# Kernel optimization log

Measured on AMD Instinct MI355X. Metric: run time of the kernel, lower is better.

Reference implementation:

```python
import jax, jax.numpy as jnp
import numpy as np
import math

HEADS, DIM_HEAD, LANDMARKS, PINV_ITERS = 8, 64, 256, 6
EMB = 512


def layer_norm(x, g, b, eps=1e-5):
    mu = jnp.mean(x, -1, keepdims=True)
    var = jnp.mean((x - mu) ** 2, -1, keepdims=True)
    return (x - mu) / jnp.sqrt(var + eps) * g + b


def moore_penrose_pinv(x, iters=PINV_ITERS):
    # iterative Moore-Penrose pseudo-inverse (lucidrains nystrom-attention)
    abs_x = jnp.abs(x)
    col = abs_x.sum(-1)
    row = abs_x.sum(-2)
    z = jnp.swapaxes(x, -1, -2) / (jnp.max(col) * jnp.max(row))
    I = jnp.eye(x.shape[-1], dtype=x.dtype)
    for _ in range(iters):
        xz = x @ z
        z = 0.25 * z @ (13.0 * I - xz @ (15.0 * I - xz @ (7.0 * I - xz)))
    return z


def dw_seq_conv(v, w):
    # v: [b, h, n, d]; depthwise Conv2d(heads, heads, (33,1), pad (16,0), groups=heads)
    return jax.lax.conv_general_dilated(
        v, w, (1, 1), ((w.shape[2] // 2, w.shape[2] // 2), (0, 0)),
        dimension_numbers=('NCHW', 'OIHW', 'NCHW'), feature_group_count=v.shape[1])


def nystrom_attention(x, qkv_w, out_w, out_b, res_w):
    b, n, _ = x.shape
    m = LANDMARKS
    pad = (m - n % m) % m
    if pad:
        x = jnp.pad(x, ((0, 0), (pad, 0), (0, 0)))  # front-pad like F.pad(..., padding, 0)
    n_p = n + pad
    qkv = x @ qkv_w  # [b, n_p, 3*h*dh]
    q, k, v = jnp.split(qkv, 3, axis=-1)
    to_h = lambda t: t.reshape(b, n_p, HEADS, DIM_HEAD).transpose(0, 2, 1, 3)
    q, k, v = to_h(q), to_h(k), to_h(v)
    q = q * (DIM_HEAD ** -0.5)
    l = n_p // m  # tokens per landmark
    q_l = q.reshape(b, HEADS, m, l, DIM_HEAD).mean(3)
    k_l = k.reshape(b, HEADS, m, l, DIM_HEAD).mean(3)
    a1 = jax.nn.softmax(jnp.einsum('bhid,bhjd->bhij', q, k_l), -1)    # [b,h,n_p,m]
    a2 = jax.nn.softmax(jnp.einsum('bhid,bhjd->bhij', q_l, k_l), -1)  # [b,h,m,m]
    a3 = jax.nn.softmax(jnp.einsum('bhid,bhjd->bhij', q_l, k), -1)    # [b,h,m,n_p]
    a2_inv = moore_penrose_pinv(a2)
    out = (a1 @ a2_inv) @ (a3 @ v)  # [b,h,n_p,dh]
    out = out + dw_seq_conv(v, res_w)  # residual depthwise conv on v
    out = out.transpose(0, 2, 1, 3).reshape(b, n_p, HEADS * DIM_HEAD)
    out = out @ out_w + out_b
    return out[:, -n:]


def ppeg(x, H, W, w7, b7, w5, b5, w3, b3):
    B, _, C = x.shape
    cls_t, feat = x[:, :1], x[:, 1:]
    f = feat.transpose(0, 2, 1).reshape(B, C, H, W)
    def dw(w, b):
        y = jax.lax.conv_general_dilated(
            f, w, (1, 1), 'SAME', dimension_numbers=('NCHW', 'OIHW', 'NCHW'),
            feature_group_count=C)
        return y + b[None, :, None, None]
    y = f + dw(w7, b7) + dw(w5, b5) + dw(w3, b3)
    y = y.reshape(B, C, H * W).transpose(0, 2, 1)
    return jnp.concatenate([cls_t, y], axis=1)


def setup_inputs():
    key = jax.random.key(0)
    ks = jax.random.split(key, 20)
    rn = lambda k, shp, s=0.02: jax.random.normal(k, shp, jnp.float32) * s
    return {
        'x_path': jax.random.normal(ks[0], (4, 6000, 1024), jnp.float32),
        'fc1_w': rn(ks[1], (1024, EMB)), 'fc1_b': jnp.zeros((EMB,), jnp.float32),
        'cls_token': jax.random.normal(ks[2], (1, 1, EMB), jnp.float32),
        'ln1_g': jnp.ones((EMB,), jnp.float32), 'ln1_b': jnp.zeros((EMB,), jnp.float32),
        'qkv1_w': rn(ks[3], (EMB, 3 * HEADS * DIM_HEAD)),
        'out1_w': rn(ks[4], (HEADS * DIM_HEAD, EMB)), 'out1_b': jnp.zeros((EMB,), jnp.float32),
        'res1_w': rn(ks[5], (HEADS, 1, 33, 1)),
        'ln2_g': jnp.ones((EMB,), jnp.float32), 'ln2_b': jnp.zeros((EMB,), jnp.float32),
        'qkv2_w': rn(ks[6], (EMB, 3 * HEADS * DIM_HEAD)),
        'out2_w': rn(ks[7], (HEADS * DIM_HEAD, EMB)), 'out2_b': jnp.zeros((EMB,), jnp.float32),
        'res2_w': rn(ks[8], (HEADS, 1, 33, 1)),
        'conv7_w': rn(ks[9], (EMB, 1, 7, 7)), 'conv7_b': jnp.zeros((EMB,), jnp.float32),
        'conv5_w': rn(ks[10], (EMB, 1, 5, 5)), 'conv5_b': jnp.zeros((EMB,), jnp.float32),
        'conv3_w': rn(ks[11], (EMB, 1, 3, 3)), 'conv3_b': jnp.zeros((EMB,), jnp.float32),
        'norm_g': jnp.ones((EMB,), jnp.float32), 'norm_b': jnp.zeros((EMB,), jnp.float32),
        'fc2_w': rn(ks[12], (EMB, 4)), 'fc2_b': jnp.zeros((4,), jnp.float32),
    }


def reference(x_path, fc1_w, fc1_b, cls_token, ln1_g, ln1_b, qkv1_w, out1_w, out1_b,
              res1_w, ln2_g, ln2_b, qkv2_w, out2_w, out2_b, res2_w,
              conv7_w, conv7_b, conv5_w, conv5_b, conv3_w, conv3_b,
              norm_g, norm_b, fc2_w, fc2_b):
    h = jax.nn.relu(x_path @ fc1_w + fc1_b)  # [B, N, EMB]
    B, N = h.shape[0], h.shape[1]
    _H = int(math.ceil(math.sqrt(N)))
    add = _H * _H - N
    h = jnp.concatenate([h, h[:, :add]], axis=1)            # square padding
    cls = jnp.broadcast_to(cls_token, (B, 1, EMB))
    h = jnp.concatenate([cls, h], axis=1)                   # [B, _H*_H+1, EMB]
    # TransLayer 1
    h = h + nystrom_attention(layer_norm(h, ln1_g, ln1_b), qkv1_w, out1_w, out1_b, res1_w)
    # PPEG positional encoding
    h = ppeg(h, _H, _H, conv7_w, conv7_b, conv5_w, conv5_b, conv3_w, conv3_b)
    # TransLayer 2
    h = h + nystrom_attention(layer_norm(h, ln2_g, ln2_b), qkv2_w, out2_w, out2_b, res2_w)
    h = layer_norm(h, norm_g, norm_b)
    logits = h @ fc2_w + fc2_b
    cls_logit = logits[:, 0]
    Y_hat = jnp.argmax(cls_logit, axis=1)
    hazards = jax.nn.sigmoid(cls_logit)
    S = jnp.cumprod(1.0 - hazards, axis=1)
    return hazards, S, Y_hat
```

## Files before the change

### kernel.cpp

```cpp
#include <hip/hip_runtime.h>
#include <math.h>

namespace {

constexpr int Bq   = 4;
constexpr int N0   = 6000;
constexpr int KIN  = 1024;
constexpr int E    = 512;
constexpr int HH   = 78;
constexpr int HWp  = 6084;
constexpr int N1   = 6085;
constexpr int NH   = 8;
constexpr int DH   = 64;
constexpr int LM   = 256;
constexpr int NP   = 6144;
constexpr int LCH  = 24;
constexpr int PADS = 59;
constexpr int BH   = Bq * NH;
constexpr int QKV  = 3 * E;
constexpr int NSPL = 8;

typedef __attribute__((ext_vector_type(8))) short bf16x8;
typedef __attribute__((ext_vector_type(4))) float f32x4;

// ... 140 lines not shown
          float vv = (wch == 0) ? v * 0.125f : v;
          unsigned short* dst = (wch == 0) ? qp : (wch == 1) ? kp : vp;
          dst[(((size_t)(b * NH + hd)) * NP + p) * DH + d] = f2bf(vv);
        } else if (STORE == 1) {
          C[((size_t)(row / N0) * N1 + 1 + (row % N0)) * N + col] = v;
        } else if (STORE == 3) {
          C[(size_t)row * N + col] += v;
        } else {
          C[(size_t)row * N + col] = v;
        }
      }
    }
  }
}

template<bool WN, bool WT, bool TBF>
__global__ __launch_bounds__(256)
void mm_ns(const float* __restrict__ A, const float* __restrict__ BT,
           float* __restrict__ Cn, unsigned short* __restrict__ CtB,
           float* __restrict__ CtF, int Ncols, int Mtot, int K,
           long long sA, long long sBT, long long sCn, long long sCt,
           float cN, float aN, float cT, float aT)
{
  int bx = blockIdx.x, by = blockIdx.y, bz = blockIdx.z;
  {
    const int gx = gridDim.x, gy = gridDim.y;
    int nid = xcd_swz((bz * gy + by) * gx + bx, gx * gy * gridDim.z);
    bx = nid % gx; nid /= gx; by = nid % gy; bz = nid / gy;
  }
  A  += (size_t)bz * sA;
  BT += (size_t)bz * sBT;
  __shared__ __align__(16) char smem[32768];
  unsigned short* Ah = (unsigned short*)smem;
  unsigned short* Al = Ah + 4096;
  unsigned short* Bh = Ah + 8192;
  unsigned short* Bl = Ah + 12288;
  const int t = threadIdx.x, lane = t & 63, w = t >> 6;
  const int l15 = lane & 15, g = lane >> 4;
  const int rb = by * 64, cb = bx * 64;
  const int wr = w * 16;

  f32x4 acc[4];
  #pragma unroll
  for (int ni = 0; ni < 4; ni++) acc[ni] = (f32x4){0.f, 0.f, 0.f, 0.f};

  for (int k0 = 0; k0 < K; k0 += 64) {
    if (k0) __syncthreads();
    #pragma unroll
    for (int it = 0; it < 4; it++) {
      const int id = it * 256 + t;
      const int row = id >> 4, kq = (id & 15) * 4;
      float4 va = *reinterpret_cast<const float4*>(A + (size_t)(rb + row) * K + k0 + kq);
      const int eo = row * 64 + swz8(row, kq >> 3) * 8 + (kq & 7);
      unsigned short h0 = f2bf(va.x), h1 = f2bf(va.y), h2 = f2bf(va.z), h3 = f2bf(va.w);
      unsigned short lo0 = f2bf(va.x - bf2f(h0)), lo1 = f2bf(va.y - bf2f(h1));
      unsigned short lo2 = f2bf(va.z - bf2f(h2)), lo3 = f2bf(va.w - bf2f(h3));
      *reinterpret_cast<ushort4*>(&Ah[eo]) = make_ushort4(h0, h1, h2, h3);
      *reinterpret_cast<ushort4*>(&Al[eo]) = make_ushort4(lo0, lo1, lo2, lo3);
      float4 vb = *reinterpret_cast<const float4*>(BT + (size_t)(cb + row) * K + k0 + kq);
      unsigned short b0 = f2bf(vb.x), b1 = f2bf(vb.y), b2 = f2bf(vb.z), b3 = f2bf(vb.w);
      unsigned short c0_ = f2bf(vb.x - bf2f(b0)), c1 = f2bf(vb.y - bf2f(b1));
      unsigned short c2 = f2bf(vb.z - bf2f(b2)), c3 = f2bf(vb.w - bf2f(b3));
      *reinterpret_cast<ushort4*>(&Bh[eo]) = make_ushort4(b0, b1, b2, b3);
      *reinterpret_cast<ushort4*>(&Bl[eo]) = make_ushort4(c0_, c1, c2, c3);
    }
    __syncthreads();
    #pragma unroll
    for (int ds = 0; ds < 2; ds++) {
      const int ar = wr + l15;
      bf16x8 ah = *reinterpret_cast<const bf16x8*>(&Ah[ar * 64 + swz8(ar, ds * 4 + g) * 8]);
      bf16x8 al = *reinterpret_cast<const bf16x8*>(&Al[ar * 64 + swz8(ar, ds * 4 + g) * 8]);
      #pragma unroll
      for (int ni = 0; ni < 4; ni++) {
        const int nr = ni * 16 + l15;
        bf16x8 bhf = *reinterpret_cast<const bf16x8*>(&Bh[nr * 64 + swz8(nr, ds * 4 + g) * 8]);
        bf16x8 blf = *reinterpret_cast<const bf16x8*>(&Bl[nr * 64 + swz8(nr, ds * 4 + g) * 8]);
        acc[ni] = __builtin_amdgcn_mfma_f32_16x16x32_bf16(ah, bhf, acc[ni], 0, 0, 0);
        acc[ni] = __builtin_amdgcn_mfma_f32_16x16x32_bf16(ah, blf, acc[ni], 0, 0, 0);
        acc[ni] = __builtin_amdgcn_mfma_f32_16x16x32_bf16(al, bhf, acc[ni], 0, 0, 0);
      }
    }
  }
  __syncthreads();
  float* tb = (float*)smem;
  #pragma unroll
  for (int ni = 0; ni < 4; ni++)
    #pragma unroll
    for (int r = 0; r < 4; r++)
      tb[(wr + g * 4 + r) * 65 + l15 + ni * 16] = acc[ni][r];
  __syncthreads();
  #pragma unroll
  for (int it = 0; it < 4; it++) {
    const int id = it * 256 + t;
    const int row = id >> 4, q4 = (id & 15) * 4;
    if (WN) {
      float4 o;
      #pragma unroll
      for (int j = 0; j < 4; j++) {
        float v = tb[row * 65 + q4 + j];
        ((float*)&o)[j] = ((rb + row) == (cb + q4 + j) ? cN : 0.f) + aN * v;
      }
      *reinterpret_cast<float4*>(Cn + (size_t)bz * sCn + (size_t)(rb + row) * Ncols + cb + q4) = o;
    }
    if (WT) {
      float v[4];
      #pragma unroll
      for (int j = 0; j < 4; j++) {
        float m = tb[(q4 + j) * 65 + row];
        v[j] = ((cb + row) == (rb + q4 + j) ? cT : 0.f) + aT * m;
      }
      if (TBF) {
        ushort4 o = make_ushort4(f2bf(v[0]), f2bf(v[1]), f2bf(v[2]), f2bf(v[3]));
        *reinterpret_cast<ushort4*>(CtB + (size_t)bz * sCt + (size_t)(cb + row) * Mtot + rb + q4) = o;
      } else {
        float4 o = make_float4(v[0], v[1], v[2], v[3]);
        *reinterpret_cast<float4*>(CtF + (size_t)bz * sCt + (size_t)(cb + row) * Mtot + rb + q4) = o;
      }
    }
  }
}

__global__ __launch_bounds__(256)
void a2_fused(const unsigned short* __restrict__ ql, const unsigned short* __restrict__ kl,
              float* __restrict__ a2, float* __restrict__ a2T)
{
  const int bh = blockIdx.y;
  const int t = threadIdx.x, lane = t & 63, w = t >> 6;
  const int l15 = lane & 15, g = lane >> 4;
  const int row0 = blockIdx.x * 64 + w * 16;
  __shared__ float tb[4][16][68];

  bf16x8 af[2];
// ... 147 lines not shown
  for (int r = 0; r < 4; r++) {
    const int row = lm0 + w * 16 + g * 4 + r;
    const size_t base = ((size_t)(bh * NSPL + sp) * LM + row);
    #pragma unroll
    for (int ni = 0; ni < 4; ni++)
      Opart[base * 64 + ni * 16 + l15] = O[ni][r];
    if (l15 == 0) {
      msd[base * 2]     = m[r];
      msd[base * 2 + 1] = sd[r];
    }
  }
}

__global__ __launch_bounds__(256)
void flash_a3_merge(const float* __restrict__ Opart, const float* __restrict__ msd,
                    float* __restrict__ a3vT)
{
  const int bh = blockIdx.y, lm0 = blockIdx.x * 64;
  const int t = threadIdx.x;
  const int r = t >> 2, dg = t & 3;
  const int row = lm0 + r;
  float m8[NSPL], w8[NSPL];
  float M = -INFINITY;
  #pragma unroll
  for (int s = 0; s < NSPL; s++) {
    m8[s] = msd[((size_t)(bh * NSPL + s) * LM + row) * 2];
    M = fmaxf(M, m8[s]);
  }
  float S = 0.f;
  #pragma unroll
  for (int s = 0; s < NSPL; s++) {
// ... 7 lines not shown
  for (int j = 0; j < 16; j++) acc[j] = 0.f;
  #pragma unroll
  for (int s = 0; s < NSPL; s++) {
    const float* op = Opart + ((size_t)(bh * NSPL + s) * LM + row) * 64 + dg * 16;
    #pragma unroll
    for (int j = 0; j < 16; j++) acc[j] = fmaf(w8[s], op[j], acc[j]);
  }
  __shared__ float Tl[64][65];
  #pragma unroll
  for (int j = 0; j < 16; j++) Tl[dg * 16 + j][r] = acc[j] * invS;
  __syncthreads();
  const int d = t >> 2, q4 = t & 3;
  #pragma unroll
  for (int j = 0; j < 4; j++) {
    const int c0 = q4 * 16 + j * 4;
    float4 o = make_float4(Tl[d][c0], Tl[d][c0 + 1], Tl[d][c0 + 2], Tl[d][c0 + 3]);
    *reinterpret_cast<float4*>(a3vT + ((size_t)bh * 64 + d) * 256 + lm0 + c0) = o;
  }
}

__global__ __launch_bounds__(256)
void a1_fused(const unsigned short* __restrict__ q, const unsigned short* __restrict__ kl,
              const unsigned short* __restrict__ W2T, const unsigned short* __restrict__ v,
              const float* __restrict__ resw, unsigned short* __restrict__ heads)
{
  const int bh = blockIdx.y;
  const int p0 = blockIdx.x * 64;
  const int t = threadIdx.x, lane = t & 63, w = t >> 6;
  const int l15 = lane & 15, g = lane >> 4;
  __shared__ __align__(16) unsigned short Pl[4][4096];
  __shared__ __align__(16) unsigned short VTc[8192];
  __shared__ __align__(16) unsigned short P2[8192];

  const float* w33 = resw + (bh & 7) * 33;
  for (int i = t; i < 64 * 96; i += 256) {
    const int r = i / 96, kk = i % 96;
    const int d = kk - r;
    const float val = (d >= 0 && d <= 32) ? w33[d] : 0.f;
    P2[r * 128 + swz8(r, kk >> 3) * 8 + (kk & 7)] = f2bf(val);
  }
  #pragma unroll
  for (int it = 0; it < 3; it++) {
    const int id = it * 256 + t;
    const int kp = id >> 3, ch = id & 7;
    const int gp = p0 - 16 + kp;
    int4 vv = make_int4(0, 0, 0, 0);
    if (gp >= 0 && gp < NP)
      vv = *reinterpret_cast<const int4*>(v + ((size_t)bh * NP + gp) * 64 + ch * 8);
    const unsigned short* ps = (const unsigned short*)&vv;
    #pragma unroll
    for (int j = 0; j < 8; j++) {
      const int d = ch * 8 + j;
      VTc[d * 128 + swz8(d, kp >> 3) * 8 + (kp & 7)] = ps[j];
    }
  }
// ... 17 lines not shown
  for (int r = 0; r < 4; r++) {
    float m = -INFINITY;
    #pragma unroll
    for (int ni = 0; ni < 16; ni++) m = fmaxf(m, s[ni][r]);
    #pragma unroll
    for (int msk = 1; msk < 16; msk <<= 1) m = fmaxf(m, __shfl_xor(m, msk));
    float sm = 0.f;
    #pragma unroll
    for (int ni = 0; ni < 16; ni++) { float e = expf(s[ni][r] - m); s[ni][r] = e; sm += e; }
    #pragma unroll
    for (int msk = 1; msk < 16; msk <<= 1) sm += __shfl_xor(sm, msk);
    const float inv = 1.f / sm;
    #pragma unroll
    for (int ni = 0; ni < 16; ni++) s[ni][r] *= inv;
  }
  unsigned short* Pw = Pl[w];
  #pragma unroll
  for (int ni = 0; ni < 16; ni++)
    #pragma unroll
    for (int r = 0; r < 4; r++) {
      const int rowl = g * 4 + r, col = ni * 16 + l15;
      Pw[rowl * 256 + swz8(rowl, col >> 3) * 8 + (col & 7)] = f2bf(s[ni][r]);
    }
  f32x4 O[4];
  #pragma unroll
  for (int ni = 0; ni < 4; ni++) O[ni] = (f32x4){0.f, 0.f, 0.f, 0.f};
  #pragma unroll
  for (int ks = 0; ks < 8; ks++) {
    bf16x8 pa = *reinterpret_cast<const bf16x8*>(&Pw[l15 * 256 + swz8(l15, ks * 4 + g) * 8]);
    #pragma unroll
    for (int ni = 0; ni < 4; ni++) {
      bf16x8 bf = *reinterpret_cast<const bf16x8*>(
          W2T + ((size_t)bh * 64 + ni * 16 + l15) * 256 + ks * 32 + g * 8);
      O[ni] = __builtin_amdgcn_mfma_f32_16x16x32_bf16(pa, bf, O[ni], 0, 0, 0);
    }
  }
  #pragma unroll
  for (int ks = 0; ks < 3; ks++) {
    const int ar = w * 16 + l15;
    bf16x8 pa = *reinterpret_cast<const bf16x8*>(&P2[ar * 128 + swz8(ar, ks * 4 + g) * 8]);
    #pragma unroll
    for (int ni = 0; ni < 4; ni++) {
      const int d = ni * 16 + l15;
      bf16x8 bv = *reinterpret_cast<const bf16x8*>(&VTc[d * 128 + swz8(d, ks * 4 + g) * 8]);
      O[ni] = __builtin_amdgcn_mfma_f32_16x16x32_bf16(pa, bv, O[ni], 0, 0, 0);
    }
  }
  #pragma unroll
  for (int ni = 0; ni < 4; ni++)
    #pragma unroll
    for (int r = 0; r < 4; r++)
      heads[((size_t)bh * NP + p0 + w * 16 + g * 4 + r) * 64 + ni * 16 + l15] = f2bf(O[ni][r]);
}

__global__ __launch_bounds__(256)
void ln_stats(const float* __restrict__ X, float* __restrict__ stats)
{
  const size_t row = blockIdx.x;
  const float* x = X + row * E;
  const int tid = threadIdx.x;
  float2 v = *reinterpret_cast<const float2*>(x + tid * 2);
  __shared__ float red[256];
  red[tid] = v.x + v.y;
  __syncthreads();
  for (int s = 128; s > 0; s >>= 1) { if (tid < s) red[tid] += red[tid + s]; __syncthreads(); }
  const float mu = red[0] * (1.f / E);
  __syncthreads();
  const float dx = v.x - mu, dy = v.y - mu;
  red[tid] = dx * dx + dy * dy;
  __syncthreads();
  for (int s = 128; s > 0; s >>= 1) { if (tid < s) red[tid] += red[tid + s]; __syncthreads(); }
  if (tid == 0) {
    stats[2 * row]     = mu;
    stats[2 * row + 1] = 1.f / sqrtf(red[0] * (1.f / E) + 1e-5f);
  }
}

__global__ __launch_bounds__(256)
void ln_to_bf16(const float* __restrict__ h, const float* __restrict__ stats,
                const float* __restrict__ g, const float* __restrict__ b,
                unsigned short* __restrict__ xb)
{
  long long idx = (long long)blockIdx.x * 256 + threadIdx.x;
  const long long total = (long long)Bq * N1 * (E / 4);
  if (idx >= total) return;
  const int e4 = (int)(idx % (E / 4));
  const long long row = idx / (E / 4);
  float4 hx = reinterpret_cast<const float4*>(h)[idx];
  const float mu = stats[2 * row], inv = stats[2 * row + 1];
  float4 gg = reinterpret_cast<const float4*>(g)[e4];
  float4 bb = reinterpret_cast<const float4*>(b)[e4];
  ushort4 o;
  o.x = f2bf((hx.x - mu) * inv * gg.x + bb.x);
  o.y = f2bf((hx.y - mu) * inv * gg.y + bb.y);
  o.z = f2bf((hx.z - mu) * inv * gg.z + bb.z);
  o.w = f2bf((hx.w - mu) * inv * gg.w + bb.w);
  reinterpret_cast<ushort4*>(xb)[idx] = o;
}

__global__ void fill_cls_wrap(const float* __restrict__ cls, float* __restrict__ h)
{
  int idx = blockIdx.x * 256 + threadIdx.x;
  const int total = Bq * 85 * (E / 4);
  if (idx >= total) return;
  const int e4 = idx % (E / 4);
  int t = idx / (E / 4);
  const int rr = t % 85;
  const int b = t / 85;
  float4* H = reinterpret_cast<float4*>(h);
  if (rr == 0) {
    H[((size_t)b * N1) * (E / 4) + e4] = reinterpret_cast<const float4*>(cls)[e4];
  } else {
    const int i = rr - 1;
    H[((size_t)b * N1 + 1 + N0 + i) * (E / 4) + e4] =
        H[((size_t)b * N1 + 1 + i) * (E / 4) + e4];
  }
}

__global__ __launch_bounds__(256)
void landmark_mean(const float* __restrict__ h, const float* __restrict__ stats,
                   const float* __restrict__ g, const float* __restrict__ bta,
                   unsigned short* __restrict__ xl)
{
  const int bm = blockIdx.x;
  const int b = bm / LM, i = bm % LM;
  const int tid = threadIdx.x;
  float2 acc = make_float2(0.f, 0.f);
  float cnt = 0.f;
  for (int j = 0; j < LCH; j++) {
    const int real = i * LCH + j - PADS;
    if (real < 0) continue;
    const size_t row = (size_t)b * N1 + real;
    float2 hv = *reinterpret_cast<const float2*>(h + row * E + tid * 2);
    const float mu = stats[2 * row], inv = stats[2 * row + 1];
    acc.x += (hv.x - mu) * inv;
    acc.y += (hv.y - mu) * inv;
    cnt += 1.f;
  }
  float2 gg = *reinterpret_cast<const float2*>(g + tid * 2);
  float2 bb = *reinterpret_cast<const float2*>(bta + tid * 2);
  ushort2 o;
  o.x = f2bf((gg.x * acc.x + bb.x * cnt) * (1.f / LCH));
  o.y = f2bf((gg.y * acc.y + bb.y * cnt) * (1.f / LCH));
  *reinterpret_cast<ushort2*>(xl + (size_t)bm * E + tid * 2) = o;
}

__global__ void zero_pad_rows(unsigned short* __restrict__ q, unsigned short* __restrict__ k,
                              unsigned short* __restrict__ v)
{
  const int idx = blockIdx.x * 256 + threadIdx.x;
  const int total = BH * PADS * DH;
  if (idx >= total) return;
  const int d = idx % DH;
  int t = idx / DH;
  const int p = t % PADS;
  const int bh = t / PADS;
  const size_t o = ((size_t)bh * NP + p) * DH + d;
  q[o] = 0; k[o] = 0; v[o] = 0;
// ... 30 lines not shown
  for (int j = 0; j < LM; j++) rowsum += a[(size_t)tid * LM + j];
  for (int i = 0; i < LM; i++) colsum += a[(size_t)i * LM + tid];
  __shared__ float r1[256], r2[256];
  r1[tid] = rowsum; r2[tid] = colsum;
  __syncthreads();
  for (int s = 128; s > 0; s >>= 1) {
    if (tid < s) { r1[tid] = fmaxf(r1[tid], r1[tid + s]); r2[tid] = fmaxf(r2[tid], r2[tid + s]); }
    __syncthreads();
  }
  if (tid == 0) {
    atomicMax(&gmax[0], __float_as_uint(r1[0]));
    atomicMax(&gmax[1], __float_as_uint(r2[0]));
  }
}

__global__ void pinv_init2(const float* __restrict__ a2, const float* __restrict__ a2T,
                           const unsigned int* __restrict__ gmax,
                           float* __restrict__ zA, float* __restrict__ zAT)
{
  long long idx = (long long)blockIdx.x * 256 + threadIdx.x;
  const long long total = (long long)BH * LM * LM;
  if (idx >= total) return;
  const float inv = 1.f / (__uint_as_float(gmax[0]) * __uint_as_float(gmax[1]));
  zA[idx]  = a2T[idx] * inv;
  zAT[idx] = a2[idx] * inv;
}

__global__ __launch_bounds__(256)
void last_row_attn(const unsigned short* __restrict__ q, const unsigned short* __restrict__ kl,
                   const unsigned short* __restrict__ W2T, const unsigned short* __restrict__ v,
                   const float* __restrict__ resw, float* __restrict__ hb)
{
  const int bh = blockIdx.x;
  const int tid = threadIdx.x;
  __shared__ float qrow[DH];
  __shared__ float p[LM];
  __shared__ float red[256];
  if (tid < DH) qrow[tid] = bf2f(q[((size_t)bh * NP + PADS) * DH + tid]);
  __syncthreads();
  const unsigned short* krow = kl + ((size_t)bh * LM + tid) * DH;
// ... 199 lines not shown
    for (int j = 1; j < 4; j++) if (lg[j] > bvv) { bvv = lg[j]; best = j; }
    float S = 1.f;
    for (int j = 0; j < 4; j++) {
      const float hz = 1.f / (1.f + expf(-lg[j]));
      out[b * 4 + j] = hz;
      S *= (1.f - hz);
      out[16 + b * 4 + j] = S;
    }
    out[32 + b] = (float)best;
  }
}

__global__ void write_sentinel(float* out) { if (threadIdx.x < 36) out[threadIdx.x] = -777.f; }

struct Ws {
  unsigned short *q, *k, *v, *ql, *kl, *xl, *W2T;
  unsigned short *fc1T, *qkv1T, *qkv2T, *out1T;
  float *h, *pool, *a3vT, *qkvl, *stats;
  unsigned int* gmax;
};

constexpr long long MM = (long long)BH * LM * LM;

static void run_attention(hipStream_t stream, Ws& w,
                          const float* lng, const float* lnb, const unsigned short* qkvT,
                          const unsigned short* outT, const float* outb, const float* resw,
                          bool last)
{
  const dim3 blk(256);
  float* a2   = w.pool;
  float* a2T  = w.pool + MM;
  float* zA   = w.pool + 2 * MM;
  float* zAT  = w.pool + 3 * MM;
  float* zB   = w.pool + 4 * MM;
  float* zBT  = w.pool + 5 * MM;
  float* Y    = w.pool + 6 * MM;
  float* P1T  = w.pool + 7 * MM;
  float* P2T  = w.pool + 8 * MM;
  float* P3T  = w.pool + 9 * MM;
  unsigned short* xb    = (unsigned short*)w.pool;
  unsigned short* heads = (unsigned short*)(w.pool + 6 * MM);
  float* Opart = w.pool + 6 * MM;
  float* msd   = w.pool + 6 * MM + (long long)BH * NSPL * LM * DH;
  float* hb = w.qkvl;

  ln_stats<<<Bq * N1, blk, 0, stream>>>(w.h, w.stats);
  ln_to_bf16<<<gblocks_i((long long)Bq * N1 * (E / 4)), blk, 0, stream>>>(w.h, w.stats, lng, lnb, xb);
  landmark_mean<<<Bq * LM, blk, 0, stream>>>(w.h, w.stats, lng, lnb, w.xl);
  mgemm<3, 2, false, false, true><<<dim3(QKV / 128, (Bq * N1 + 127) / 128), blk, 0, stream>>>(
      xb, qkvT, nullptr, nullptr, w.q, w.k, w.v, nullptr, Bq * N1, QKV, E);
  zero_pad_rows<<<gblocks_i((long long)BH * PADS * DH), blk, 0, stream>>>(w.q, w.k, w.v);
  mgemm<3, 0, false, false, false><<<dim3(8, 8), blk, 0, stream>>>(
      w.xl, qkvT, nullptr, w.qkvl, nullptr, nullptr, nullptr, nullptr, Bq * LM, 1024, E);
  scatter_qk_l<<<gblocks_i((long long)Bq * LM * 256), blk, 0, stream>>>(w.qkvl, w.ql, w.kl);

  a2_fused<<<dim3(4, BH), blk, 0, stream>>>(w.ql, w.kl, a2, a2T);
  init_gmax<<<1, 64, 0, stream>>>(w.gmax);
  colrow_max<<<BH, blk, 0, stream>>>(a2, w.gmax);
  pinv_init2<<<gblocks_i(MM), blk, 0, stream>>>(a2, a2T, w.gmax, zA, zAT);

  float *zc = zA, *zcT = zAT, *zo = zB, *zoT = zBT;
  const long long sM = (long long)LM * LM;
  for (int it = 0; it < 6; ++it) {
    mm_ns<true, true, false><<<dim3(4, 4, BH), blk, 0, stream>>>(
        a2, zcT, Y, nullptr, P1T, 256, 256, 256, sM, sM, sM, sM, 0.f, 1.f, 7.f, -1.f);
    mm_ns<false, true, false><<<dim3(4, 4, BH), blk, 0, stream>>>(
        Y, P1T, nullptr, nullptr, P2T, 256, 256, 256, sM, sM, sM, sM, 0.f, 0.f, 15.f, -1.f);
    mm_ns<false, true, false><<<dim3(4, 4, BH), blk, 0, stream>>>(
        Y, P2T, nullptr, nullptr, P3T, 256, 256, 256, sM, sM, sM, sM, 0.f, 0.f, 13.f, -1.f);
    mm_ns<true, true, false><<<dim3(4, 4, BH), blk, 0, stream>>>(
        zc, P3T, zo, nullptr, zoT, 256, 256, 256, sM, sM, sM, sM, 0.f, 0.25f, 0.f, 0.25f);
    float* t1 = zc; zc = zo; zo = t1;
    float* t2 = zcT; zcT = zoT; zoT = t2;
  }

  flash_a3_split<<<dim3(4, NSPL, BH), blk, 0, stream>>>(w.ql, w.k, w.v, Opart, msd);
  flash_a3_merge<<<dim3(4, BH), blk, 0, stream>>>(Opart, msd, w.a3vT);
  mm_ns<false, true, true><<<dim3(1, 4, BH), blk, 0, stream>>>(
      zc, w.a3vT, nullptr, w.W2T, nullptr, 64, 256, 256, sM, 64 * 256, 0, 64 * 256,
      0.f, 0.f, 0.f, 1.f);

  if (!last) {
    a1_fused<<<dim3(NP / 64, BH), blk, 0, stream>>>(w.q, w.kl, w.W2T, w.v, resw, heads);
    mgemm<4, 3, true, false, true><<<dim3(E / 128, (Bq * N1 + 127) / 128), blk, 0, stream>>>(
        nullptr, outT, outb, w.h, nullptr, nullptr, nullptr, heads, Bq * N1, E, E);
  } else {
    last_row_attn<<<BH, blk, 0, stream>>>(w.q, w.kl, w.W2T, w.v, resw, hb);
  }
}

}

extern "C" void kernel_launch(void* const* d_in, const int* in_sizes, int n_in,
                              void* d_out, int out_size, void* d_ws, size_t ws_size,
                              hipStream_t stream)
{
  const float* x_path   = (const float*)d_in[0];
  const float* fc1_w    = (const float*)d_in[1];
  const float* fc1_b    = (const float*)d_in[2];
  const float* cls_tok  = (const float*)d_in[3];
  const float* ln1_g    = (const float*)d_in[4];
  const float* ln1_b    = (const float*)d_in[5];
// ... 21 lines not shown

  float* W = (float*)d_ws;
  size_t off = 0;
  auto take = [&](size_t n) -> float* {
    float* p = W + off;
    off += (n + 255) & ~(size_t)255;
    return p;
  };

  Ws w;
  w.q     = (unsigned short*)take((size_t)BH * NP * DH / 2);
  w.k     = (unsigned short*)take((size_t)BH * NP * DH / 2);
  w.v     = (unsigned short*)take((size_t)BH * NP * DH / 2);
  w.h     = take((size_t)Bq * N1 * E);
  w.pool  = take((size_t)10 * MM);
  w.a3vT  = take((size_t)BH * DH * LM);
  w.W2T   = (unsigned short*)take((size_t)BH * DH * LM / 2);
  w.ql    = (unsigned short*)take((size_t)BH * LM * DH / 2);
  w.kl    = (unsigned short*)take((size_t)BH * LM * DH / 2);
  w.xl    = (unsigned short*)take((size_t)Bq * LM * E / 2);
  w.qkvl  = take((size_t)Bq * LM * 1024);
  w.stats = take((size_t)2 * Bq * N1);
  w.fc1T  = (unsigned short*)take((size_t)E * KIN / 2);
  w.qkv1T = (unsigned short*)take((size_t)QKV * E / 2);
  w.qkv2T = (unsigned short*)take((size_t)QKV * E / 2);
  w.out1T = (unsigned short*)take((size_t)E * E / 2);
  w.gmax  = (unsigned int*)take(64);

  if (ws_size < off * sizeof(float)) {
    write_sentinel<<<1, 64, 0, stream>>>((float*)d_out);
    return;
  }

  const dim3 blk(256);

  wcvt_t<<<dim3(E / 32, KIN / 32), blk, 0, stream>>>(fc1_w, w.fc1T, KIN, E);
  wcvt_t<<<dim3(QKV / 32, E / 32), blk, 0, stream>>>(qkv1_w, w.qkv1T, E, QKV);
// ... 23 lines not shown
```

Baseline: 1.931 ms.

## Store pinv matrices as pre-split bf16 hi/lo pairs and fuse layernorm passes

The Newton-Schulz pinv matmuls now read and write matrices already split into bf16 high/low halves, so the fp32-to-bf16 split in every tile load is gone and global traffic is smaller. LayerNorm stats and the bf16 conversion are merged into one kernel, and landmark means are taken from the normalized bf16 output rather than recomputed from fp32. a1_fused loads its depthwise-conv band matrix from a buffer built once per layer, and writes its P tile to shared memory in two halves, cutting LDS use and possibly raising occupancy. Taking landmark means from rounded bf16 values slightly changes numerics.

Measured after the change: 1.830 ms. 5.2% less time.

```diff
diff --git a/kernel.cpp b/kernel.cpp
--- a/kernel.cpp
+++ b/kernel.cpp
@@ -178,13 +178,15 @@
   }
 }
 
-template<bool WN, bool WT, bool TBF>
-__global__ __launch_bounds__(256)
-void mm_ns(const float* __restrict__ A, const float* __restrict__ BT,
-           float* __restrict__ Cn, unsigned short* __restrict__ CtB,
-           float* __restrict__ CtF, int Ncols, int Mtot, int K,
-           long long sA, long long sBT, long long sCn, long long sCt,
-           float cN, float aN, float cT, float aT)
+template<bool WN, bool WT>
+__global__ __launch_bounds__(256)
+void mm_ns2(const unsigned short* __restrict__ Ah, const unsigned short* __restrict__ Al,
+            const unsigned short* __restrict__ Bth, const unsigned short* __restrict__ Btl,
+            unsigned short* __restrict__ Cnh, unsigned short* __restrict__ Cnl,
+            unsigned short* __restrict__ Cth, unsigned short* __restrict__ Ctl,
+            int Ncols, int Mtot, int K,
+            long long sA, long long sB, long long sCn, long long sCt,
+            float cN, float aN, float cT, float aT)
 {
   int bx = blockIdx.x, by = blockIdx.y, bz = blockIdx.z;
   {
@@ -192,13 +194,15 @@
     int nid = xcd_swz((bz * gy + by) * gx + bx, gx * gy * gridDim.z);
     bx = nid % gx; nid /= gx; by = nid % gy; bz = nid / gy;
   }
-  A  += (size_t)bz * sA;
-  BT += (size_t)bz * sBT;
+  const unsigned short* Ahb = Ah + (size_t)bz * sA;
+  const unsigned short* Alb = Al + (size_t)bz * sA;
+  const unsigned short* Bhb = Bth + (size_t)bz * sB;
+  const unsigned short* Blb = Btl + (size_t)bz * sB;
   __shared__ __align__(16) char smem[32768];
-  unsigned short* Ah = (unsigned short*)smem;
-  unsigned short* Al = Ah + 4096;
-  unsigned short* Bh = Ah + 8192;
-  unsigned short* Bl = Ah + 12288;
+  unsigned short* AhS = (unsigned short*)smem;
+  unsigned short* AlS = AhS + 4096;
+  unsigned short* BhS = AhS + 8192;
+  unsigned short* BlS = AhS + 12288;
   const int t = threadIdx.x, lane = t & 63, w = t >> 6;
   const int l15 = lane & 15, g = lane >> 4;
   const int rb = by * 64, cb = bx * 64;
@@ -211,34 +215,28 @@
   for (int k0 = 0; k0 < K; k0 += 64) {
     if (k0) __syncthreads();
     #pragma unroll
-    for (int it = 0; it < 4; it++) {
+    for (int it = 0; it < 2; it++) {
       const int id = it * 256 + t;
-      const int row = id >> 4, kq = (id & 15) * 4;
-      float4 va = *reinterpret_cast<const float4*>(A + (size_t)(rb + row) * K + k0 + kq);
-      const int eo = row * 64 + swz8(row, kq >> 3) * 8 + (kq & 7);
-      unsigned short h0 = f2bf(va.x), h1 = f2bf(va.y), h2 = f2bf(va.z), h3 = f2bf(va.w);
-      unsigned short lo0 = f2bf(va.x - bf2f(h0)), lo1 = f2bf(va.y - bf2f(h1));
-      unsigned short lo2 = f2bf(va.z - bf2f(h2)), lo3 = f2bf(va.w - bf2f(h3));
-      *reinterpret_cast<ushort4*>(&Ah[eo]) = make_ushort4(h0, h1, h2, h3);
-      *reinterpret_cast<ushort4*>(&Al[eo]) = make_ushort4(lo0, lo1, lo2, lo3);
-      float4 vb = *reinterpret_cast<const float4*>(BT + (size_t)(cb + row) * K + k0 + kq);
-      unsigned short b0 = f2bf(vb.x), b1 = f2bf(vb.y), b2 = f2bf(vb.z), b3 = f2bf(vb.w);
-      unsigned short c0_ = f2bf(vb.x - bf2f(b0)), c1 = f2bf(vb.y - bf2f(b1));
-      unsigned short c2 = f2bf(vb.z - bf2f(b2)), c3 = f2bf(vb.w - bf2f(b3));
-      *reinterpret_cast<ushort4*>(&Bh[eo]) = make_ushort4(b0, b1, b2, b3);
-      *reinterpret_cast<ushort4*>(&Bl[eo]) = make_ushort4(c0_, c1, c2, c3);
+      const int row = id >> 3, ch = id & 7;
+      const int eo = row * 64 + swz8(row, ch) * 8;
+      const size_t ga = (size_t)(rb + row) * K + k0 + ch * 8;
+      const size_t gb = (size_t)(cb + row) * K + k0 + ch * 8;
+      *reinterpret_cast<int4*>(&AhS[eo]) = *reinterpret_cast<const int4*>(Ahb + ga);
+      *reinterpret_cast<int4*>(&AlS[eo]) = *reinterpret_cast<const int4*>(Alb + ga);
+      *reinterpret_cast<int4*>(&BhS[eo]) = *reinterpret_cast<const int4*>(Bhb + gb);
+      *reinterpret_cast<int4*>(&BlS[eo]) = *reinterpret_cast<const int4*>(Blb + gb);
     }
     __syncthreads();
     #pragma unroll
     for (int ds = 0; ds < 2; ds++) {
       const int ar = wr + l15;
-      bf16x8 ah = *reinterpret_cast<const bf16x8*>(&Ah[ar * 64 + swz8(ar, ds * 4 + g) * 8]);
-      bf16x8 al = *reinterpret_cast<const bf16x8*>(&Al[ar * 64 + swz8(ar, ds * 4 + g) * 8]);
+      bf16x8 ah = *reinterpret_cast<const bf16x8*>(&AhS[ar * 64 + swz8(ar, ds * 4 + g) * 8]);
+      bf16x8 al = *reinterpret_cast<const bf16x8*>(&AlS[ar * 64 + swz8(ar, ds * 4 + g) * 8]);
       #pragma unroll
       for (int ni = 0; ni < 4; ni++) {
         const int nr = ni * 16 + l15;
-        bf16x8 bhf = *reinterpret_cast<const bf16x8*>(&Bh[nr * 64 + swz8(nr, ds * 4 + g) * 8]);
-        bf16x8 blf = *reinterpret_cast<const bf16x8*>(&Bl[nr * 64 + swz8(nr, ds * 4 + g) * 8]);
+        bf16x8 bhf = *reinterpret_cast<const bf16x8*>(&BhS[nr * 64 + swz8(nr, ds * 4 + g) * 8]);
+        bf16x8 blf = *reinterpret_cast<const bf16x8*>(&BlS[nr * 64 + swz8(nr, ds * 4 + g) * 8]);
         acc[ni] = __builtin_amdgcn_mfma_f32_16x16x32_bf16(ah, bhf, acc[ni], 0, 0, 0);
         acc[ni] = __builtin_amdgcn_mfma_f32_16x16x32_bf16(ah, blf, acc[ni], 0, 0, 0);
         acc[ni] = __builtin_amdgcn_mfma_f32_16x16x32_bf16(al, bhf, acc[ni], 0, 0, 0);
@@ -258,28 +256,30 @@
     const int id = it * 256 + t;
     const int row = id >> 4, q4 = (id & 15) * 4;
     if (WN) {
-      float4 o;
+      ushort4 oh, ol;
       #pragma unroll
       for (int j = 0; j < 4; j++) {
-        float v = tb[row * 65 + q4 + j];
-        ((float*)&o)[j] = ((rb + row) == (cb + q4 + j) ? cN : 0.f) + aN * v;
-      }
-      *reinterpret_cast<float4*>(Cn + (size_t)bz * sCn + (size_t)(rb + row) * Ncols + cb + q4) = o;
+        const float v = ((rb + row) == (cb + q4 + j) ? cN : 0.f) + aN * tb[row * 65 + q4 + j];
+        const unsigned short h = f2bf(v);
+        ((unsigned short*)&oh)[j] = h;
+        ((unsigned short*)&ol)[j] = f2bf(v - bf2f(h));
+      }
+      const size_t o = (size_t)bz * sCn + (size_t)(rb + row) * Ncols + cb + q4;
+      *reinterpret_cast<ushort4*>(Cnh + o) = oh;
+      *reinterpret_cast<ushort4*>(Cnl + o) = ol;
     }
     if (WT) {
-      float v[4];
+      ushort4 oh, ol;
       #pragma unroll
       for (int j = 0; j < 4; j++) {
-        float m = tb[(q4 + j) * 65 + row];
-        v[j] = ((cb + row) == (rb + q4 + j) ? cT : 0.f) + aT * m;
-      }
-      if (TBF) {
-        ushort4 o = make_ushort4(f2bf(v[0]), f2bf(v[1]), f2bf(v[2]), f2bf(v[3]));
-        *reinterpret_cast<ushort4*>(CtB + (size_t)bz * sCt + (size_t)(cb + row) * Mtot + rb + q4) = o;
-      } else {
-        float4 o = make_float4(v[0], v[1], v[2], v[3]);
-        *reinterpret_cast<float4*>(CtF + (size_t)bz * sCt + (size_t)(cb + row) * Mtot + rb + q4) = o;
-      }
+        const float v = ((cb + row) == (rb + q4 + j) ? cT : 0.f) + aT * tb[(q4 + j) * 65 + row];
+        const unsigned short h = f2bf(v);
+        ((unsigned short*)&oh)[j] = h;
+        ((unsigned short*)&ol)[j] = f2bf(v - bf2f(h));
+      }
+      const size_t o = (size_t)bz * sCt + (size_t)(cb + row) * Mtot + rb + q4;
+      *reinterpret_cast<ushort4*>(Cth + o) = oh;
+      *reinterpret_cast<ushort4*>(Ctl + o) = ol;
     }
   }
 }
@@ -457,7 +457,7 @@
 
 __global__ __launch_bounds__(256)
 void flash_a3_merge(const float* __restrict__ Opart, const float* __restrict__ msd,
-                    float* __restrict__ a3vT)
+                    unsigned short* __restrict__ a3vTh, unsigned short* __restrict__ a3vTl)
 {
   const int bh = blockIdx.y, lm0 = blockIdx.x * 64;
   const int t = threadIdx.x;
@@ -495,31 +495,44 @@
   #pragma unroll
   for (int j = 0; j < 4; j++) {
     const int c0 = q4 * 16 + j * 4;
-    float4 o = make_float4(Tl[d][c0], Tl[d][c0 + 1], Tl[d][c0 + 2], Tl[d][c0 + 3]);
-    *reinterpret_cast<float4*>(a3vT + ((size_t)bh * 64 + d) * 256 + lm0 + c0) = o;
+    ushort4 oh, ol;
+    #pragma unroll
+    for (int jj = 0; jj < 4; jj++) {
+      const float v = Tl[d][c0 + jj];
+      const unsigned short h = f2bf(v);
+      ((unsigned short*)&oh)[jj] = h;
+      ((unsigned short*)&ol)[jj] = f2bf(v - bf2f(h));
+    }
+    const size_t o = ((size_t)bh * 64 + d) * 256 + lm0 + c0;
+    *reinterpret_cast<ushort4*>(a3vTh + o) = oh;
+    *reinterpret_cast<ushort4*>(a3vTl + o) = ol;
+  }
+}
+
+__global__ __launch_bounds__(256)
+void build_band(const float* __restrict__ resw, unsigned short* __restrict__ P2g)
+{
+  const int head = blockIdx.x;
+  const float* w33 = resw + head * 33;
+  for (int i = threadIdx.x; i < 64 * 96; i += 256) {
+    const int r = i / 96, kk = i % 96;
+    const int d = kk - r;
+    P2g[(size_t)head * 64 * 96 + i] = f2bf((d >= 0 && d <= 32) ? w33[d] : 0.f);
   }
 }
 
 __global__ __launch_bounds__(256)
 void a1_fused(const unsigned short* __restrict__ q, const unsigned short* __restrict__ kl,
               const unsigned short* __restrict__ W2T, const unsigned short* __restrict__ v,
-              const float* __restrict__ resw, unsigned short* __restrict__ heads)
+              const unsigned short* __restrict__ P2g, unsigned short* __restrict__ heads)
 {
   const int bh = blockIdx.y;
   const int p0 = blockIdx.x * 64;
   const int t = threadIdx.x, lane = t & 63, w = t >> 6;
   const int l15 = lane & 15, g = lane >> 4;
-  __shared__ __align__(16) unsigned short Pl[4][4096];
   __shared__ __align__(16) unsigned short VTc[8192];
-  __shared__ __align__(16) unsigned short P2[8192];
-
-  const float* w33 = resw + (bh & 7) * 33;
-  for (int i = t; i < 64 * 96; i += 256) {
-    const int r = i / 96, kk = i % 96;
-    const int d = kk - r;
-    const float val = (d >= 0 && d <= 32) ? w33[d] : 0.f;
-    P2[r * 128 + swz8(r, kk >> 3) * 8 + (kk & 7)] = f2bf(val);
-  }
+  __shared__ __align__(16) unsigned short Pl[4][2048];
+
   #pragma unroll
   for (int it = 0; it < 3; it++) {
     const int id = it * 256 + t;
@@ -567,31 +580,39 @@
     #pragma unroll
     for (int ni = 0; ni < 16; ni++) s[ni][r] *= inv;
   }
+
+  f32x4 O[4];
+  #pragma unroll
+  for (int ni = 0; ni < 4; ni++) O[ni] = (f32x4){0.f, 0.f, 0.f, 0.f};
   unsigned short* Pw = Pl[w];
   #pragma unroll
-  for (int ni = 0; ni < 16; ni++)
-    #pragma unroll
-    for (int r = 0; r < 4; r++) {
-      const int rowl = g * 4 + r, col = ni * 16 + l15;
-      Pw[rowl * 256 + swz8(rowl, col >> 3) * 8 + (col & 7)] = f2bf(s[ni][r]);
-    }
-  f32x4 O[4];
-  #pragma unroll
-  for (int ni = 0; ni < 4; ni++) O[ni] = (f32x4){0.f, 0.f, 0.f, 0.f};
-  #pragma unroll
-  for (int ks = 0; ks < 8; ks++) {
-    bf16x8 pa = *reinterpret_cast<const bf16x8*>(&Pw[l15 * 256 + swz8(l15, ks * 4 + g) * 8]);
-    #pragma unroll
-    for (int ni = 0; ni < 4; ni++) {
-      bf16x8 bf = *reinterpret_cast<const bf16x8*>(
-          W2T + ((size_t)bh * 64 + ni * 16 + l15) * 256 + ks * 32 + g * 8);
-      O[ni] = __builtin_amdgcn_mfma_f32_16x16x32_bf16(pa, bf, O[ni], 0, 0, 0);
-    }
-  }
+  for (int hf = 0; hf < 2; hf++) {
+    #pragma unroll
+    for (int ni2 = 0; ni2 < 8; ni2++)
+      #pragma unroll
+      for (int r = 0; r < 4; r++) {
+        const int rowl = g * 4 + r, col = ni2 * 16 + l15;
+        Pw[rowl * 128 + swz8(rowl, col >> 3) * 8 + (col & 7)] = f2bf(s[hf * 8 + ni2][r]);
+      }
+    __asm__ __volatile__("" ::: "memory");
+    #pragma unroll
+    for (int ks2 = 0; ks2 < 4; ks2++) {
+      const int ks = hf * 4 + ks2;
+      bf16x8 pa = *reinterpret_cast<const bf16x8*>(&Pw[l15 * 128 + swz8(l15, ks2 * 4 + g) * 8]);
+      #pragma unroll
+      for (int ni = 0; ni < 4; ni++) {
+        bf16x8 bf = *reinterpret_cast<const bf16x8*>(
+            W2T + ((size_t)bh * 64 + ni * 16 + l15) * 256 + ks * 32 + g * 8);
+        O[ni] = __builtin_amdgcn_mfma_f32_16x16x32_bf16(pa, bf, O[ni], 0, 0, 0);
+      }
+    }
+    __asm__ __volatile__("" ::: "memory");
+  }
+  const unsigned short* band = P2g + (size_t)(bh & 7) * 64 * 96;
   #pragma unroll
   for (int ks = 0; ks < 3; ks++) {
     const int ar = w * 16 + l15;
-    bf16x8 pa = *reinterpret_cast<const bf16x8*>(&P2[ar * 128 + swz8(ar, ks * 4 + g) * 8]);
+    bf16x8 pa = *reinterpret_cast<const bf16x8*>(band + (size_t)ar * 96 + ks * 32 + g * 8);
     #pragma unroll
     for (int ni = 0; ni < 4; ni++) {
       const int d = ni * 16 + l15;
@@ -607,7 +628,8 @@
 }
 
 __global__ __launch_bounds__(256)
-void ln_stats(const float* __restrict__ X, float* __restrict__ stats)
+void ln_fused(const float* __restrict__ X, const float* __restrict__ g,
+              const float* __restrict__ b, unsigned short* __restrict__ xb)
 {
   const size_t row = blockIdx.x;
   const float* x = X + row * E;
@@ -623,32 +645,13 @@
   red[tid] = dx * dx + dy * dy;
   __syncthreads();
   for (int s = 128; s > 0; s >>= 1) { if (tid < s) red[tid] += red[tid + s]; __syncthreads(); }
-  if (tid == 0) {
-    stats[2 * row]     = mu;
-    stats[2 * row + 1] = 1.f / sqrtf(red[0] * (1.f / E) + 1e-5f);
-  }
-}
-
-__global__ __launch_bounds__(256)
-void ln_to_bf16(const float* __restrict__ h, const float* __restrict__ stats,
-                const float* __restrict__ g, const float* __restrict__ b,
-                unsigned short* __restrict__ xb)
-{
-  long long idx = (long long)blockIdx.x * 256 + threadIdx.x;
-  const long long total = (long long)Bq * N1 * (E / 4);
-  if (idx >= total) return;
-  const int e4 = (int)(idx % (E / 4));
-  const long long row = idx / (E / 4);
-  float4 hx = reinterpret_cast<const float4*>(h)[idx];
-  const float mu = stats[2 * row], inv = stats[2 * row + 1];
-  float4 gg = reinterpret_cast<const float4*>(g)[e4];
-  float4 bb = reinterpret_cast<const float4*>(b)[e4];
-  ushort4 o;
-  o.x = f2bf((hx.x - mu) * inv * gg.x + bb.x);
-  o.y = f2bf((hx.y - mu) * inv * gg.y + bb.y);
-  o.z = f2bf((hx.z - mu) * inv * gg.z + bb.z);
-  o.w = f2bf((hx.w - mu) * inv * gg.w + bb.w);
-  reinterpret_cast<ushort4*>(xb)[idx] = o;
+  const float inv = 1.f / sqrtf(red[0] * (1.f / E) + 1e-5f);
+  float2 gg = *reinterpret_cast<const float2*>(g + tid * 2);
+  float2 bb = *reinterpret_cast<const float2*>(b + tid * 2);
+  ushort2 o;
+  o.x = f2bf(dx * inv * gg.x + bb.x);
+  o.y = f2bf(dy * inv * gg.y + bb.y);
+  *reinterpret_cast<ushort2*>(xb + row * E + tid * 2) = o;
 }
 
 __global__ void fill_cls_wrap(const float* __restrict__ cls, float* __restrict__ h)
@@ -671,30 +674,22 @@
 }
 
 __global__ __launch_bounds__(256)
-void landmark_mean(const float* __restrict__ h, const float* __restrict__ stats,
-                   const float* __restrict__ g, const float* __restrict__ bta,
-                   unsigned short* __restrict__ xl)
+void landmark_mean(const unsigned short* __restrict__ xb, unsigned short* __restrict__ xl)
 {
   const int bm = blockIdx.x;
   const int b = bm / LM, i = bm % LM;
   const int tid = threadIdx.x;
   float2 acc = make_float2(0.f, 0.f);
-  float cnt = 0.f;
   for (int j = 0; j < LCH; j++) {
     const int real = i * LCH + j - PADS;
     if (real < 0) continue;
-    const size_t row = (size_t)b * N1 + real;
-    float2 hv = *reinterpret_cast<const float2*>(h + row * E + tid * 2);
-    const float mu = stats[2 * row], inv = stats[2 * row + 1];
-    acc.x += (hv.x - mu) * inv;
-    acc.y += (hv.y - mu) * inv;
-    cnt += 1.f;
-  }
-  float2 gg = *reinterpret_cast<const float2*>(g + tid * 2);
-  float2 bb = *reinterpret_cast<const float2*>(bta + tid * 2);
+    ushort2 hv = *reinterpret_cast<const ushort2*>(xb + ((size_t)b * N1 + real) * E + tid * 2);
+    acc.x += bf2f(hv.x);
+    acc.y += bf2f(hv.y);
+  }
   ushort2 o;
-  o.x = f2bf((gg.x * acc.x + bb.x * cnt) * (1.f / LCH));
-  o.y = f2bf((gg.y * acc.y + bb.y * cnt) * (1.f / LCH));
+  o.x = f2bf(acc.x * (1.f / LCH));
+  o.y = f2bf(acc.y * (1.f / LCH));
   *reinterpret_cast<ushort2*>(xl + (size_t)bm * E + tid * 2) = o;
 }
 
@@ -755,16 +750,25 @@
   }
 }
 
-__global__ void pinv_init2(const float* __restrict__ a2, const float* __restrict__ a2T,
+__global__ void pinv_init3(const float* __restrict__ a2, const float* __restrict__ a2T,
                            const unsigned int* __restrict__ gmax,
-                           float* __restrict__ zA, float* __restrict__ zAT)
+                           unsigned short* __restrict__ a2h, unsigned short* __restrict__ a2l,
+                           unsigned short* __restrict__ znh, unsigned short* __restrict__ znl,
+                           unsigned short* __restrict__ zth, unsigned short* __restrict__ ztl)
 {
   long long idx = (long long)blockIdx.x * 256 + threadIdx.x;
   const long long total = (long long)BH * LM * LM;
   if (idx >= total) return;
   const float inv = 1.f / (__uint_as_float(gmax[0]) * __uint_as_float(gmax[1]));
-  zA[idx]  = a2T[idx] * inv;
-  zAT[idx] = a2[idx] * inv;
+  const float a = a2[idx];
+  unsigned short h = f2bf(a);
+  a2h[idx] = h; a2l[idx] = f2bf(a - bf2f(h));
+  const float z = a2T[idx] * inv;
+  h = f2bf(z);
+  znh[idx] = h; znl[idx] = f2bf(z - bf2f(h));
+  const float zt = a * inv;
+  h = f2bf(zt);
+  zth[idx] = h; ztl[idx] = f2bf(zt - bf2f(h));
 }
 
 __global__ __launch_bounds__(256)
@@ -994,9 +998,10 @@
 __global__ void write_sentinel(float* out) { if (threadIdx.x < 36) out[threadIdx.x] = -777.f; }
 
 struct Ws {
-  unsigned short *q, *k, *v, *ql, *kl, *xl, *W2T;
+  unsigned short *q, *k, *v, *ql, *kl, *xl;
+  unsigned short *a3vTh, *a3vTl, *W2Th, *W2Tl, *P2g;
   unsigned short *fc1T, *qkv1T, *qkv2T, *out1T;
-  float *h, *pool, *a3vT, *qkvl, *stats;
+  float *h, *pool, *qkvl;
   unsigned int* gmax;
 };
 
@@ -1008,25 +1013,29 @@
                           bool last)
 {
   const dim3 blk(256);
-  float* a2   = w.pool;
-  float* a2T  = w.pool + MM;
-  float* zA   = w.pool + 2 * MM;
-  float* zAT  = w.pool + 3 * MM;
-  float* zB   = w.pool + 4 * MM;
-  float* zBT  = w.pool + 5 * MM;
-  float* Y    = w.pool + 6 * MM;
-  float* P1T  = w.pool + 7 * MM;
-  float* P2T  = w.pool + 8 * MM;
-  float* P3T  = w.pool + 9 * MM;
-  unsigned short* xb    = (unsigned short*)w.pool;
-  unsigned short* heads = (unsigned short*)(w.pool + 6 * MM);
-  float* Opart = w.pool + 6 * MM;
-  float* msd   = w.pool + 6 * MM + (long long)BH * NSPL * LM * DH;
+  char* P = (char*)w.pool;
+  float* a2f  = (float*)P;
+  float* a2Tf = (float*)(P + MM * 4);
+  unsigned short* a2h = (unsigned short*)(P + MM * 8);
+  unsigned short* a2l = (unsigned short*)(P + MM * 10);
+  unsigned short* zA[4] = { (unsigned short*)(P + MM * 12), (unsigned short*)(P + MM * 14),
+                            (unsigned short*)(P + MM * 16), (unsigned short*)(P + MM * 18) };
+  unsigned short* zB[4] = { (unsigned short*)(P + MM * 20), (unsigned short*)(P + MM * 22),
+                            (unsigned short*)(P + MM * 24), (unsigned short*)(P + MM * 26) };
+  unsigned short* Yh = (unsigned short*)(P + MM * 28);
+  unsigned short* Yl = (unsigned short*)(P + MM * 30);
+  unsigned short* Uh = (unsigned short*)(P + MM * 32);
+  unsigned short* Ul = (unsigned short*)(P + MM * 34);
+  unsigned short* Vh = (unsigned short*)(P + MM * 36);
+  unsigned short* Vl = (unsigned short*)(P + MM * 38);
+  unsigned short* xb = (unsigned short*)P;
+  float* Opart = (float*)(P + MM * 28);
+  float* msd   = (float*)(P + MM * 28 + (long long)BH * NSPL * LM * DH * 4);
+  unsigned short* heads = (unsigned short*)(P + MM * 20);
   float* hb = w.qkvl;
 
-  ln_stats<<<Bq * N1, blk, 0, stream>>>(w.h, w.stats);
-  ln_to_bf16<<<gblocks_i((long long)Bq * N1 * (E / 4)), blk, 0, stream>>>(w.h, w.stats, lng, lnb, xb);
-  landmark_mean<<<Bq * LM, blk, 0, stream>>>(w.h, w.stats, lng, lnb, w.xl);
+  ln_fused<<<Bq * N1, blk, 0, stream>>>(w.h, lng, lnb, xb);
+  landmark_mean<<<Bq * LM, blk, 0, stream>>>(xb, w.xl);
   mgemm<3, 2, false, false, true><<<dim3(QKV / 128, (Bq * N1 + 127) / 128), blk, 0, stream>>>(
       xb, qkvT, nullptr, nullptr, w.q, w.k, w.v, nullptr, Bq * N1, QKV, E);
   zero_pad_rows<<<gblocks_i((long long)BH * PADS * DH), blk, 0, stream>>>(w.q, w.k, w.v);
@@ -1034,38 +1043,43 @@
       w.xl, qkvT, nullptr, w.qkvl, nullptr, nullptr, nullptr, nullptr, Bq * LM, 1024, E);
   scatter_qk_l<<<gblocks_i((long long)Bq * LM * 256), blk, 0, stream>>>(w.qkvl, w.ql, w.kl);
 
-  a2_fused<<<dim3(4, BH), blk, 0, stream>>>(w.ql, w.kl, a2, a2T);
+  a2_fused<<<dim3(4, BH), blk, 0, stream>>>(w.ql, w.kl, a2f, a2Tf);
   init_gmax<<<1, 64, 0, stream>>>(w.gmax);
-  colrow_max<<<BH, blk, 0, stream>>>(a2, w.gmax);
-  pinv_init2<<<gblocks_i(MM), blk, 0, stream>>>(a2, a2T, w.gmax, zA, zAT);
-
-  float *zc = zA, *zcT = zAT, *zo = zB, *zoT = zBT;
+  colrow_max<<<BH, blk, 0, stream>>>(a2f, w.gmax);
+  pinv_init3<<<gblocks_i(MM), blk, 0, stream>>>(a2f, a2Tf, w.gmax, a2h, a2l,
+                                                zA[0], zA[1], zA[2], zA[3]);
+
+  unsigned short **zc = zA, **zo = zB;
   const long long sM = (long long)LM * LM;
   for (int it = 0; it < 6; ++it) {
-    mm_ns<true, true, false><<<dim3(4, 4, BH), blk, 0, stream>>>(
-        a2, zcT, Y, nullptr, P1T, 256, 256, 256, sM, sM, sM, sM, 0.f, 1.f, 7.f, -1.f);
-    mm_ns<false, true, false><<<dim3(4, 4, BH), blk, 0, stream>>>(
-        Y, P1T, nullptr, nullptr, P2T, 256, 256, 256, sM, sM, sM, sM, 0.f, 0.f, 15.f, -1.f);
-    mm_ns<false, true, false><<<dim3(4, 4, BH), blk, 0, stream>>>(
-        Y, P2T, nullptr, nullptr, P3T, 256, 256, 256, sM, sM, sM, sM, 0.f, 0.f, 13.f, -1.f);
-    mm_ns<true, true, false><<<dim3(4, 4, BH), blk, 0, stream>>>(
-        zc, P3T, zo, nullptr, zoT, 256, 256, 256, sM, sM, sM, sM, 0.f, 0.25f, 0.f, 0.25f);
-    float* t1 = zc; zc = zo; zo = t1;
-    float* t2 = zcT; zcT = zoT; zoT = t2;
+    mm_ns2<true, true><<<dim3(4, 4, BH), blk, 0, stream>>>(
+        a2h, a2l, zc[2], zc[3], Yh, Yl, Uh, Ul,
+        256, 256, 256, sM, sM, sM, sM, 0.f, 1.f, 7.f, -1.f);
+    mm_ns2<false, true><<<dim3(4, 4, BH), blk, 0, stream>>>(
+        Yh, Yl, Uh, Ul, nullptr, nullptr, Vh, Vl,
+        256, 256, 256, sM, sM, sM, sM, 0.f, 0.f, 15.f, -1.f);
+    mm_ns2<false, true><<<dim3(4, 4, BH), blk, 0, stream>>>(
+        Yh, Yl, Vh, Vl, nullptr, nullptr, Uh, Ul,
+        256, 256, 256, sM, sM, sM, sM, 0.f, 0.f, 13.f, -1.f);
+    mm_ns2<true, true><<<dim3(4, 4, BH), blk, 0, stream>>>(
+        zc[0], zc[1], Uh, Ul, zo[0], zo[1], zo[2], zo[3],
+        256, 256, 256, sM, sM, sM, sM, 0.f, 0.25f, 0.f, 0.25f);
+    unsigned short** tp = zc; zc = zo; zo = tp;
   }
 
   flash_a3_split<<<dim3(4, NSPL, BH), blk, 0, stream>>>(w.ql, w.k, w.v, Opart, msd);
-  flash_a3_merge<<<dim3(4, BH), blk, 0, stream>>>(Opart, msd, w.a3vT);
-  mm_ns<false, true, true><<<dim3(1, 4, BH), blk, 0, stream>>>(
-      zc, w.a3vT, nullptr, w.W2T, nullptr, 64, 256, 256, sM, 64 * 256, 0, 64 * 256,
-      0.f, 0.f, 0.f, 1.f);
+  flash_a3_merge<<<dim3(4, BH), blk, 0, stream>>>(Opart, msd, w.a3vTh, w.a3vTl);
+  mm_ns2<false, true><<<dim3(1, 4, BH), blk, 0, stream>>>(
+      zc[0], zc[1], w.a3vTh, w.a3vTl, nullptr, nullptr, w.W2Th, w.W2Tl,
+      64, 256, 256, sM, 64 * 256, 0, 64 * 256, 0.f, 0.f, 0.f, 1.f);
 
   if (!last) {
-    a1_fused<<<dim3(NP / 64, BH), blk, 0, stream>>>(w.q, w.kl, w.W2T, w.v, resw, heads);
+    build_band<<<NH, blk, 0, stream>>>(resw, w.P2g);
+    a1_fused<<<dim3(NP / 64, BH), blk, 0, stream>>>(w.q, w.kl, w.W2Th, w.v, w.P2g, heads);
     mgemm<4, 3, true, false, true><<<dim3(E / 128, (Bq * N1 + 127) / 128), blk, 0, stream>>>(
         nullptr, outT, outb, w.h, nullptr, nullptr, nullptr, heads, Bq * N1, E, E);
   } else {
-    last_row_attn<<<BH, blk, 0, stream>>>(w.q, w.kl, w.W2T, w.v, resw, hb);
+    last_row_attn<<<BH, blk, 0, stream>>>(w.q, w.kl, w.W2Th, w.v, resw, hb);
   }
 }
 
@@ -1117,13 +1131,15 @@
   w.v     = (unsigned short*)take((size_t)BH * NP * DH / 2);
   w.h     = take((size_t)Bq * N1 * E);
   w.pool  = take((size_t)10 * MM);
-  w.a3vT  = take((size_t)BH * DH * LM);
-  w.W2T   = (unsigned short*)take((size_t)BH * DH * LM / 2);
+  w.a3vTh = (unsigned short*)take((size_t)BH * DH * LM / 2);
+  w.a3vTl = (unsigned short*)take((size_t)BH * DH * LM / 2);
+  w.W2Th  = (unsigned short*)take((size_t)BH * DH * LM / 2);
+  w.W2Tl  = (unsigned short*)take((size_t)BH * DH * LM / 2);
   w.ql    = (unsigned short*)take((size_t)BH * LM * DH / 2);
   w.kl    = (unsigned short*)take((size_t)BH * LM * DH / 2);
   w.xl    = (unsigned short*)take((size_t)Bq * LM * E / 2);
   w.qkvl  = take((size_t)Bq * LM * 1024);
-  w.stats = take((size_t)2 * Bq * N1);
+  w.P2g   = (unsigned short*)take((size_t)NH * 64 * 96 / 2 + 64);
   w.fc1T  = (unsigned short*)take((size_t)E * KIN / 2);
   w.qkv1T = (unsigned short*)take((size_t)QKV * E / 2);
   w.qkv2T = (unsigned short*)take((size_t)QKV * E / 2);
```
